# Kernel tuning notes

Hardware: AMD Instinct MI355X
Metric: run time of the kernel (lower is better)

The kernel has to match this reference:

```python
import jax, jax.numpy as jnp
import numpy as np

N_HEAD = 12
EPS_NORM = 1e-12   # F.normalize eps
EPS_DENOM = 1e-6   # clamp(min=1e-6)


def _l2norm(t):
    n = jnp.sqrt(jnp.sum(t * t, axis=-1, keepdims=True))
    return t / jnp.maximum(n, EPS_NORM)


def setup_inputs() -> dict:
    key = jax.random.key(0)
    ks = jax.random.split(key, 5)
    B, T, C = 1, 4096, 768
    x = jax.random.normal(ks[0], (B, T, C), dtype=jnp.float32)
    w_attn = jax.random.normal(ks[1], (C, 3 * C), dtype=jnp.float32) * 0.02
    b_attn = jnp.zeros((3 * C,), dtype=jnp.float32)
    w_proj = jax.random.normal(ks[2], (C, C), dtype=jnp.float32) * 0.02
    b_proj = jnp.zeros((C,), dtype=jnp.float32)
    return {"x": x, "w_attn": w_attn, "b_attn": b_attn,
            "w_proj": w_proj, "b_proj": b_proj}


def reference(x, w_attn, b_attn, w_proj, b_proj):
    B, T, C = x.shape
    H = N_HEAD
    hd = C // H
    qkv = x @ w_attn + b_attn                      # [B,T,3C]
    q, k, v = jnp.split(qkv, 3, axis=-1)
    # [B,T,C] -> [B,H,T,hd]
    def to_heads(t):
        return t.reshape(B, T, H, hd).transpose(0, 2, 1, 3)
    q, k, v = to_heads(q), to_heads(k), to_heads(v)
    # T > 512 branch: normalized-qk cumulative linear attention
    q = _l2norm(q)
    k = _l2norm(k)
    num = jnp.einsum('bhqd,bhkd->bhqk', q, k)      # [B,H,T,T]
    denom = jnp.maximum(jnp.cumsum(num, axis=-1), EPS_DENOM)
    att = num / denom
    y = jnp.einsum('bhqk,bhkd->bhqd', att, v)      # [B,H,T,hd]
    y = y.transpose(0, 2, 1, 3).reshape(B, T, C)
    return y @ w_proj + b_proj
```

## Files before the change

### kernel.cpp

```cpp
#include <hip/hip_runtime.h>

#define T_SEQ 4096
#define H_NUM 12
#define HD    64
#define C_DIM 768
#define N_QKV 2304
#define HT    (T_SEQ * HD)

typedef float    f32x4 __attribute__((ext_vector_type(4)));
typedef _Float16 half8 __attribute__((ext_vector_type(8)));
typedef _Float16 half4 __attribute__((ext_vector_type(4)));

#define GLDS(gp, lp) __builtin_amdgcn_global_load_lds( \
    (const __attribute__((address_space(1))) void*)(gp), \
    (__attribute__((address_space(3))) void*)(lp), 16, 0, 0)

__global__ __launch_bounds__(256) void split_x_kernel(
    const float* __restrict__ x, _Float16* __restrict__ xh,
    _Float16* __restrict__ xl, int n4)
{
    const int i = blockIdx.x * 256 + threadIdx.x;
    if (i >= n4) return;
    const float4 v = ((const float4*)x)[i];
    const float vv[4] = {v.x, v.y, v.z, v.w};
    half4 h, l;
    #pragma unroll
    for (int j = 0; j < 4; ++j) {
        const _Float16 hh = (_Float16)vv[j];
        h[j] = hh;
        l[j] = (_Float16)(vv[j] - (float)hh);
    }
    ((half4*)xh)[i] = h;
    ((half4*)xl)[i] = l;
}

__global__ __launch_bounds__(256) void split_wt_kernel(
    const float* __restrict__ W, _Float16* __restrict__ wth,
    _Float16* __restrict__ wtl)
{
    __shared__ float Ws[64][65];
    const int tid = threadIdx.x;
    const int n0 = blockIdx.x * 64, k0 = blockIdx.y * 64;
    const int lr = tid >> 4, lc = (tid & 15) << 2;
    #pragma unroll
    for (int i = 0; i < 4; ++i) {
        const float4 v = *(const float4*)(W + (size_t)(k0 + lr + i * 16) * N_QKV + n0 + lc);
        Ws[lr + i * 16][lc + 0] = v.x; Ws[lr + i * 16][lc + 1] = v.y;
        Ws[lr + i * 16][lc + 2] = v.z; Ws[lr + i * 16][lc + 3] = v.w;
    }
    __syncthreads();
    const int n = tid >> 2, ks = (tid & 3) << 4;
    half8 h0, h1, l0, l1;
    #pragma unroll
    for (int j = 0; j < 8; ++j) {
        const float v = Ws[ks + j][n];
        const _Float16 hh = (_Float16)v;
        h0[j] = hh; l0[j] = (_Float16)(v - (float)hh);
    }
    #pragma unroll
    for (int j = 0; j < 8; ++j) {
        const float v = Ws[ks + 8 + j][n];
        const _Float16 hh = (_Float16)v;
        h1[j] = hh; l1[j] = (_Float16)(v - (float)hh);
    }
    const size_t dst = (size_t)(n0 + n) * C_DIM + k0 + ks;
    *(half8*)(wth + dst) = h0; *(half8*)(wth + dst + 8) = h1;
    *(half8*)(wtl + dst) = l0; *(half8*)(wtl + dst + 8) = l1;
}

__global__ __launch_bounds__(256) void gemm_qkv_kernel(
    const _Float16* __restrict__ xh, const _Float16* __restrict__ xl,
    const _Float16* __restrict__ wth, const _Float16* __restrict__ wtl,
    const float* __restrict__ bias,
    _Float16* __restrict__ qhi, _Float16* __restrict__ qlo,
    _Float16* __restrict__ khi, _Float16* __restrict__ klo,
    _Float16* __restrict__ vt)
{
    __shared__ __align__(16) _Float16 AH[128 * 64];
    __shared__ __align__(16) _Float16 AL[128 * 64];
    __shared__ __align__(16) _Float16 BH[64 * 64];
    __shared__ __align__(16) _Float16 BL[64 * 64];
    const int tid = threadIdx.x;
    const int wv = tid >> 6, lane = tid & 63;
    const int fm = lane & 15, fg = lane >> 4;
    const int lrow = lane >> 3;
    const int lcs  = (lane & 7) ^ (lrow & 7);
    const int bx = blockIdx.x;
    const int m0 = blockIdx.y * 128;

    auto dma_chunk = [&](int c) {
        const int kc0 = c * 64;
        #pragma unroll
        for (int i = 0; i < 12; ++i) {
            const int qidx = wv * 12 + i;
            if (qidx < 16) {
                const int rg = qidx;
                GLDS(xh + (size_t)(m0 + rg * 8 + lrow) * C_DIM + kc0 + lcs * 8, &AH[rg * 512]);
            } else if (qidx < 32) {
                const int rg = qidx - 16;
                GLDS(xl + (size_t)(m0 + rg * 8 + lrow) * C_DIM + kc0 + lcs * 8, &AL[rg * 512]);
            } else if (qidx < 40) {
                const int rg = qidx - 32;
                GLDS(wth + (size_t)(bx * 64 + rg * 8 + lrow) * C_DIM + kc0 + lcs * 8, &BH[rg * 512]);
            } else {
                const int rg = qidx - 40;
                GLDS(wtl + (size_t)(bx * 64 + rg * 8 + lrow) * C_DIM + kc0 + lcs * 8, &BL[rg * 512]);
            }
        }
    };

    f32x4 acc[2][4];
    #pragma unroll
    for (int mt = 0; mt < 2; ++mt)
        #pragma unroll
        for (int ct = 0; ct < 4; ++ct) acc[mt][ct] = (f32x4){0.f, 0.f, 0.f, 0.f};

    const int swz = fm & 7;
    dma_chunk(0);
    #pragma unroll 1
    for (int c = 0; c < C_DIM / 64; ++c) {
        __syncthreads();
        half8 ah[2][2], al[2][2], bh[4][2], bl[4][2];
        #pragma unroll
        for (int mt = 0; mt < 2; ++mt) {
            const int rb = (wv * 32 + mt * 16 + fm) * 64;
            #pragma unroll
            for (int kc = 0; kc < 2; ++kc) {
                const int cb = ((kc * 4 + fg) ^ swz) * 8;
                ah[mt][kc] = *(const half8*)&AH[rb + cb];
                al[mt][kc] = *(const half8*)&AL[rb + cb];
            }
        }
        #pragma unroll
        for (int ct = 0; ct < 4; ++ct) {
            const int rb = (ct * 16 + fm) * 64;
            #pragma unroll
            for (int kc = 0; kc < 2; ++kc) {
                const int cb = ((kc * 4 + fg) ^ swz) * 8;
                bh[ct][kc] = *(const half8*)&BH[rb + cb];
                bl[ct][kc] = *(const half8*)&BL[rb + cb];
            }
        }
        __syncthreads();
        if (c + 1 < C_DIM / 64) dma_chunk(c + 1);
        #pragma unroll
        for (int mt = 0; mt < 2; ++mt)
            #pragma unroll
            for (int ct = 0; ct < 4; ++ct)
                #pragma unroll
                for (int kc = 0; kc < 2; ++kc) {
                    acc[mt][ct] = __builtin_amdgcn_mfma_f32_16x16x32_f16(ah[mt][kc], bh[ct][kc], acc[mt][ct], 0, 0, 0);
                    acc[mt][ct] = __builtin_amdgcn_mfma_f32_16x16x32_f16(ah[mt][kc], bl[ct][kc], acc[mt][ct], 0, 0, 0);
                    acc[mt][ct] = __builtin_amdgcn_mfma_f32_16x16x32_f16(al[mt][kc], bh[ct][kc], acc[mt][ct], 0, 0, 0);
                }
    }

    const int sec = bx / 12, h = bx % 12;
    const size_t hb = (size_t)h * HT;
    float bb[4];
    #pragma unroll
    for (int ct = 0; ct < 4; ++ct) bb[ct] = bias[bx * 64 + ct * 16 + fm];

    if (sec < 2) {
        _Float16* dh = (sec == 0) ? qhi : khi;
        _Float16* dl = (sec == 0) ? qlo : klo;
        #pragma unroll
        for (int mt = 0; mt < 2; ++mt)
            #pragma unroll
            for (int r = 0; r < 4; ++r) {
                float o[4];
                float ss = 0.f;
                #pragma unroll
                for (int ct = 0; ct < 4; ++ct) {
                    o[ct] = acc[mt][ct][r] + bb[ct];
                    ss += o[ct] * o[ct];
                }
                #pragma unroll
                for (int mk = 1; mk < 16; mk <<= 1) ss += __shfl_xor(ss, mk, 16);
                const float invn = 1.0f / fmaxf(sqrtf(ss), 1e-12f);
                const int t = m0 + wv * 32 + mt * 16 + fg * 4 + r;
                const size_t rb = hb + (size_t)t * HD;
                #pragma unroll
                for (int ct = 0; ct < 4; ++ct) {
                    const float v = o[ct] * invn;
                    const _Float16 vh = (_Float16)v;
                    dh[rb + ct * 16 + fm] = vh;
                    dl[rb + ct * 16 + fm] = (_Float16)(v - (float)vh);
                }
            }
    } else {
        #pragma unroll
        for (int mt = 0; mt < 2; ++mt) {
            const int t0 = m0 + wv * 32 + mt * 16 + fg * 4;
            #pragma unroll
            for (int ct = 0; ct < 4; ++ct) {
                half4 pk;
                #pragma unroll
                for (int r = 0; r < 4; ++r) pk[r] = (_Float16)(acc[mt][ct][r] + bb[ct]);
                *(half4*)(vt + hb + (size_t)(ct * 16 + fm) * T_SEQ + t0) = pk;
            }
        }
    }
}

__global__ __launch_bounds__(256) void attn_kernel(
    const _Float16* __restrict__ qhi, const _Float16* __restrict__ qlo,
    const _Float16* __restrict__ khi, const _Float16* __restrict__ klo,
    const _Float16* __restrict__ vt,  _Float16* __restrict__ ylin)
{
    __shared__ __align__(16) _Float16 KH[64 * 64];
    __shared__ __align__(16) _Float16 KL[64 * 64];
    __shared__ __align__(16) _Float16 VS[64 * 64];
    __shared__ __align__(16) _Float16 P2[64][72];

    const int tid = threadIdx.x;
    const int wv = tid >> 6, lane = tid & 63;
    const int fm = lane & 15, fg = lane >> 4;
    const int lrow = lane >> 3;
    const int lcs  = (lane & 7) ^ (lrow & 7);
    const int h = blockIdx.y, qt = blockIdx.x;
    const size_t hb = (size_t)h * HT;

    const int q = qt * 64 + wv * 16 + fm;
    half8 qf[2][2];
    #pragma unroll
    for (int kc = 0; kc < 2; ++kc) {
        const size_t off = hb + (size_t)q * HD + kc * 32 + fg * 8;
        qf[0][kc] = *(const half8*)(qhi + off);
        qf[1][kc] = *(const half8*)(qlo + off);
    }

    auto dma_tile = [&](int kt) {
        const size_t kb = hb + (size_t)kt * 64 * HD;
        const int vcol = kt * 64;
        #pragma unroll
        for (int i = 0; i < 6; ++i) {
            const int qidx = wv * 6 + i;
            const int rg = qidx & 7;
            if (qidx < 8) {
                GLDS(khi + kb + (size_t)(rg * 8 + lrow) * HD + lcs * 8, &KH[rg * 512]);
            } else if (qidx < 16) {
                GLDS(klo + kb + (size_t)(rg * 8 + lrow) * HD + lcs * 8, &KL[rg * 512]);
            } else {
                GLDS(vt + hb + (size_t)(rg * 8 + lrow) * T_SEQ + vcol + lcs * 8, &VS[rg * 512]);
            }
        }
    };

    f32x4 yacc[4];
    #pragma unroll
    for (int ct = 0; ct < 4; ++ct) yacc[ct] = (f32x4){0.f, 0.f, 0.f, 0.f};
    float carry = 0.0f;
    const int swz = fm & 7;

    dma_tile(0);
    #pragma unroll 1
    for (int kt = 0; kt < T_SEQ / 64; ++kt) {
        __syncthreads();
        half8 ka[4][2], kl[4][2], vf[4][2];
        #pragma unroll
        for (int kr = 0; kr < 4; ++kr) {
            const int rb = (kr * 16 + fm) * 64;
            #pragma unroll
            for (int kc = 0; kc < 2; ++kc) {
                const int cb = ((kc * 4 + fg) ^ swz) * 8;
                ka[kr][kc] = *(const half8*)&KH[rb + cb];
                kl[kr][kc] = *(const half8*)&KL[rb + cb];
            }
        }
        #pragma unroll
        for (int ct = 0; ct < 4; ++ct) {
            const int rb = (ct * 16 + fm) * 64;
            #pragma unroll
            for (int kc = 0; kc < 2; ++kc)
                vf[ct][kc] = *(const half8*)&VS[rb + (((kc * 4 + fg) ^ swz) * 8)];
        }
        __syncthreads();
        if (kt + 1 < T_SEQ / 64) dma_tile(kt + 1);

        f32x4 sacc[4];
        #pragma unroll
        for (int kr = 0; kr < 4; ++kr) sacc[kr] = (f32x4){0.f, 0.f, 0.f, 0.f};
        #pragma unroll
        for (int kr = 0; kr < 4; ++kr)
            #pragma unroll
            for (int kc = 0; kc < 2; ++kc) {
                sacc[kr] = __builtin_amdgcn_mfma_f32_16x16x32_f16(ka[kr][kc], qf[0][kc], sacc[kr], 0, 0, 0);
                sacc[kr] = __builtin_amdgcn_mfma_f32_16x16x32_f16(ka[kr][kc], qf[1][kc], sacc[kr], 0, 0, 0);
                sacc[kr] = __builtin_amdgcn_mfma_f32_16x16x32_f16(kl[kr][kc], qf[0][kc], sacc[kr], 0, 0, 0);
            }

        #pragma unroll
        for (int kr = 0; kr < 4; ++kr) {
            const float s0 = sacc[kr][0], s1 = sacc[kr][1];
            const float s2 = sacc[kr][2], s3 = sacc[kr][3];
            const float p1 = s0 + s1, p2 = p1 + s2, p3 = p2 + s3;
            const float u1 = __shfl_xor(p3, 16, 64);
            const float pair = p3 + u1;
            const float u2 = __shfl_xor(pair, 32, 64);
            const float tot16 = pair + u2;
            const float pref = ((fg & 1) ? u1 : 0.0f) + ((fg & 2) ? u2 : 0.0f);
            const float base = carry + pref;
            carry += tot16;
            const float a0 = s0 * __builtin_amdgcn_rcpf(fmaxf(base + s0, 1e-6f));
            const float a1 = s1 * __builtin_amdgcn_rcpf(fmaxf(base + p1, 1e-6f));
            const float a2 = s2 * __builtin_amdgcn_rcpf(fmaxf(base + p2, 1e-6f));
            const float a3 = s3 * __builtin_amdgcn_rcpf(fmaxf(base + p3, 1e-6f));
            half4 pk = {(_Float16)(a0 * 0.03125f), (_Float16)(a1 * 0.03125f),
                        (_Float16)(a2 * 0.03125f), (_Float16)(a3 * 0.03125f)};
            *(half4*)&P2[wv * 16 + fm][kr * 16 + fg * 4] = pk;
        }

        #pragma unroll
        for (int kc = 0; kc < 2; ++kc) {
            const half8 af = *(const half8*)&P2[wv * 16 + fm][kc * 32 + fg * 8];
            #pragma unroll
            for (int ct = 0; ct < 4; ++ct)
                yacc[ct] = __builtin_amdgcn_mfma_f32_16x16x32_f16(af, vf[ct][kc], yacc[ct], 0, 0, 0);
        }
    }

    #pragma unroll
    for (int ct = 0; ct < 4; ++ct)
        #pragma unroll
        for (int r = 0; r < 4; ++r) {
            const int t = qt * 64 + wv * 16 + fg * 4 + r;
            ylin[(size_t)t * C_DIM + h * HD + ct * 16 + fm] =
                (_Float16)(yacc[ct][r] * 0.0078125f);
        }
}

__global__ __launch_bounds__(256) void gemm_proj_kernel(
    const _Float16* __restrict__ A, const float* __restrict__ W,
    const float* __restrict__ bias, float* __restrict__ out)
{
    __shared__ _Float16 As[64][72];
    __shared__ _Float16 Bt[64][72];
    typedef _Float16 half2v __attribute__((ext_vector_type(2)));
    const int tid = threadIdx.x;
    const int w = tid >> 6, lane = tid & 63;
    const int m = lane & 15, g = lane >> 4;
    const int row0 = blockIdx.x << 6, col0 = blockIdx.y << 6;
    const int ar = tid >> 3, ac8 = (tid & 7) << 3;
    const int bn0 = (tid & 15) << 2, bpv = tid >> 4;
    f32x4 acc[4];
    #pragma unroll
    for (int ct = 0; ct < 4; ++ct) acc[ct] = (f32x4){0.f, 0.f, 0.f, 0.f};

    for (int kt = 0; kt < C_DIM; kt += 64) {
        half8 av0 = *(const half8*)(A + (size_t)(row0 + ar)      * C_DIM + kt + ac8);
        half8 av1 = *(const half8*)(A + (size_t)(row0 + ar + 32) * C_DIM + kt + ac8);
        float4 w0[2], w1[2];
        #pragma unroll
        for (int i = 0; i < 2; ++i) {
            const int k = kt + 2 * (bpv + 16 * i);
            w0[i] = *(const float4*)(W + (size_t)k       * C_DIM + col0 + bn0);
            w1[i] = *(const float4*)(W + (size_t)(k + 1) * C_DIM + col0 + bn0);
        }
        __syncthreads();
        *(half8*)&As[ar][ac8]      = av0;
        *(half8*)&As[ar + 32][ac8] = av1;
        #pragma unroll
        for (int i = 0; i < 2; ++i) {
            const int p = bpv + 16 * i;
            const float a_[4] = {w0[i].x, w0[i].y, w0[i].z, w0[i].w};
            const float b_[4] = {w1[i].x, w1[i].y, w1[i].z, w1[i].w};
            #pragma unroll
            for (int u = 0; u < 4; ++u) {
                half2v pk = {(_Float16)a_[u], (_Float16)b_[u]};
                *(half2v*)&Bt[bn0 + u][2 * p] = pk;
            }
        }
        __syncthreads();
        #pragma unroll
        for (int kc = 0; kc < 2; ++kc) {
            const half8 a = *(half8*)&As[w * 16 + m][kc * 32 + g * 8];
            #pragma unroll
            for (int ct = 0; ct < 4; ++ct) {
                const half8 b = *(half8*)&Bt[ct * 16 + m][kc * 32 + g * 8];
                acc[ct] = __builtin_amdgcn_mfma_f32_16x16x32_f16(a, b, acc[ct], 0, 0, 0);
            }
        }
    }
    #pragma unroll
    for (int ct = 0; ct < 4; ++ct)
        #pragma unroll
        for (int r = 0; r < 4; ++r) {
            const int t = row0 + w * 16 + g * 4 + r;
            const int n = col0 + ct * 16 + m;
            out[(size_t)t * C_DIM + n] = acc[ct][r] * 4096.0f + bias[n];
        }
}

extern "C" void kernel_launch(void* const* d_in, const int* in_sizes, int n_in,
                              void* d_out, int out_size, void* d_ws, size_t ws_size,
                              hipStream_t stream)
{
    const float* x      = (const float*)d_in[0];
    const float* w_attn = (const float*)d_in[1];
    const float* b_attn = (const float*)d_in[2];
    const float* w_proj = (const float*)d_in[3];
    const float* b_proj = (const float*)d_in[4];
    float* out = (float*)d_out;

    const size_t perQK = (size_t)H_NUM * HT;
    const size_t perX  = (size_t)T_SEQ * C_DIM;
    const size_t perW  = (size_t)N_QKV * C_DIM;
    _Float16* base = (_Float16*)d_ws;
    _Float16* xhi  = base;
    _Float16* xlo  = xhi + perX;
    _Float16* wthi = xlo + perX;
    _Float16* wtlo = wthi + perW;
    _Float16* qhi  = wtlo + perW;
    _Float16* qlo  = qhi + perQK;
    _Float16* khi  = qlo + perQK;
    _Float16* klo  = khi + perQK;
    _Float16* vtp  = klo + perQK;
    _Float16* ylin = xhi;

    split_x_kernel<<<(perX / 4 + 255) / 256, 256, 0, stream>>>(x, xhi, xlo, perX / 4);
    split_wt_kernel<<<dim3(N_QKV / 64, C_DIM / 64), 256, 0, stream>>>(w_attn, wthi, wtlo);
    gemm_qkv_kernel<<<dim3(N_QKV / 64, T_SEQ / 128), 256, 0, stream>>>(
        xhi, xlo, wthi, wtlo, b_attn, qhi, qlo, khi, klo, vtp);
    attn_kernel<<<dim3(T_SEQ / 64, H_NUM), 256, 0, stream>>>(
        qhi, qlo, khi, klo, vtp, ylin);
    gemm_proj_kernel<<<dim3(T_SEQ / 64, C_DIM / 64), 256, 0, stream>>>(
        ylin, w_proj, b_proj, out);
}
```

Before: 360.7 us.

## Split key range across waves using precomputed prefix key sums

Adds a kernel that computes per-head prefix sums of K over 64-key tiles. The attention kernel uses these to get each wave's starting cumulative denominator as q·Kprefix, so the four waves handle different key ranges in parallel over all 64 queries instead of each wave walking all 4096 keys serially. Partial outputs are reduced through LDS at the end. The cost is dropping the shared-memory K/V staging and DMA prefetch in favour of direct global loads, plus higher register pressure from the 4x4 accumulator arrays.

```diff
diff --git a/kernel.cpp b/kernel.cpp
--- a/kernel.cpp
+++ b/kernel.cpp
@@ -203,131 +203,204 @@
     }
 }
 
-__global__ __launch_bounds__(256) void attn_kernel(
+__global__ __launch_bounds__(1024) void ksp_kernel(
+    const _Float16* __restrict__ khi, const _Float16* __restrict__ klo,
+    _Float16* __restrict__ ksphi, _Float16* __restrict__ ksplo)
+{
+    __shared__ float TS[64][64];
+    const int h = blockIdx.x;
+    const int d = threadIdx.x & 63, seg = threadIdx.x >> 6;
+    const _Float16* bh = khi + (size_t)h * HT;
+    const _Float16* bl = klo + (size_t)h * HT;
+    #pragma unroll 1
+    for (int j = 0; j < 4; ++j) {
+        const int kt = seg * 4 + j;
+        float s = 0.f;
+        #pragma unroll 4
+        for (int k = 0; k < 64; ++k) {
+            const size_t key = (size_t)kt * 64 + k;
+            s += (float)bh[key * HD + d] + (float)bl[key * HD + d];
+        }
+        TS[kt][d] = s;
+    }
+    __syncthreads();
+    if (threadIdx.x < 64) {
+        float cum = 0.f;
+        #pragma unroll 1
+        for (int kt = 0; kt < 64; ++kt) {
+            const _Float16 hi = (_Float16)cum;
+            const size_t o = ((size_t)h * 64 + kt) * 64 + d;
+            ksphi[o] = hi;
+            ksplo[o] = (_Float16)(cum - (float)hi);
+            cum += TS[kt][d];
+        }
+    }
+}
+
+__global__ __launch_bounds__(256, 2) void attn_kernel(
     const _Float16* __restrict__ qhi, const _Float16* __restrict__ qlo,
     const _Float16* __restrict__ khi, const _Float16* __restrict__ klo,
-    const _Float16* __restrict__ vt,  _Float16* __restrict__ ylin)
-{
-    __shared__ __align__(16) _Float16 KH[64 * 64];
-    __shared__ __align__(16) _Float16 KL[64 * 64];
-    __shared__ __align__(16) _Float16 VS[64 * 64];
-    __shared__ __align__(16) _Float16 P2[64][72];
-
+    const _Float16* __restrict__ vt,
+    const _Float16* __restrict__ ksphi, const _Float16* __restrict__ ksplo,
+    _Float16* __restrict__ ylin)
+{
+    __shared__ __align__(16) _Float16 P2[4][64][72];
     const int tid = threadIdx.x;
     const int wv = tid >> 6, lane = tid & 63;
     const int fm = lane & 15, fg = lane >> 4;
-    const int lrow = lane >> 3;
-    const int lcs  = (lane & 7) ^ (lrow & 7);
     const int h = blockIdx.y, qt = blockIdx.x;
     const size_t hb = (size_t)h * HT;
 
-    const int q = qt * 64 + wv * 16 + fm;
-    half8 qf[2][2];
-    #pragma unroll
-    for (int kc = 0; kc < 2; ++kc) {
-        const size_t off = hb + (size_t)q * HD + kc * 32 + fg * 8;
-        qf[0][kc] = *(const half8*)(qhi + off);
-        qf[1][kc] = *(const half8*)(qlo + off);
-    }
-
-    auto dma_tile = [&](int kt) {
-        const size_t kb = hb + (size_t)kt * 64 * HD;
-        const int vcol = kt * 64;
-        #pragma unroll
-        for (int i = 0; i < 6; ++i) {
-            const int qidx = wv * 6 + i;
-            const int rg = qidx & 7;
-            if (qidx < 8) {
-                GLDS(khi + kb + (size_t)(rg * 8 + lrow) * HD + lcs * 8, &KH[rg * 512]);
-            } else if (qidx < 16) {
-                GLDS(klo + kb + (size_t)(rg * 8 + lrow) * HD + lcs * 8, &KL[rg * 512]);
-            } else {
-                GLDS(vt + hb + (size_t)(rg * 8 + lrow) * T_SEQ + vcol + lcs * 8, &VS[rg * 512]);
-            }
-        }
-    };
-
-    f32x4 yacc[4];
-    #pragma unroll
-    for (int ct = 0; ct < 4; ++ct) yacc[ct] = (f32x4){0.f, 0.f, 0.f, 0.f};
-    float carry = 0.0f;
-    const int swz = fm & 7;
-
-    dma_tile(0);
+    half8 qf[4][2][2];
+    #pragma unroll
+    for (int s = 0; s < 4; ++s)
+        #pragma unroll
+        for (int kc = 0; kc < 2; ++kc) {
+            const size_t off = hb + (size_t)(qt * 64 + s * 16 + fm) * HD + kc * 32 + fg * 8;
+            qf[s][0][kc] = *(const half8*)(qhi + off);
+            qf[s][1][kc] = *(const half8*)(qlo + off);
+        }
+
+    f32x4 basv[4];
+    {
+        const _Float16* sh = ksphi + (size_t)h * 4096;
+        const _Float16* sl = ksplo + (size_t)h * 4096;
+        #pragma unroll
+        for (int kr = 0; kr < 4; ++kr) {
+            half8 kh_[2], kl_[2];
+            #pragma unroll
+            for (int kc = 0; kc < 2; ++kc) {
+                const size_t o = (size_t)(kr * 16 + fm) * 64 + kc * 32 + fg * 8;
+                kh_[kc] = *(const half8*)(sh + o);
+                kl_[kc] = *(const half8*)(sl + o);
+            }
+            #pragma unroll
+            for (int s = 0; s < 4; ++s) {
+                f32x4 b = (f32x4){0.f, 0.f, 0.f, 0.f};
+                #pragma unroll
+                for (int kc = 0; kc < 2; ++kc) {
+                    b = __builtin_amdgcn_mfma_f32_16x16x32_f16(kh_[kc], qf[s][0][kc], b, 0, 0, 0);
+                    b = __builtin_amdgcn_mfma_f32_16x16x32_f16(kh_[kc], qf[s][1][kc], b, 0, 0, 0);
+                    b = __builtin_amdgcn_mfma_f32_16x16x32_f16(kl_[kc], qf[s][0][kc], b, 0, 0, 0);
+                }
+                basv[s][kr] = (wv == 0) ? b[0] : (wv == 1) ? b[1] : (wv == 2) ? b[2] : b[3];
+            }
+        }
+    }
+
+    f32x4 yacc[4][4];
+    #pragma unroll
+    for (int s = 0; s < 4; ++s)
+        #pragma unroll
+        for (int ct = 0; ct < 4; ++ct) yacc[s][ct] = (f32x4){0.f, 0.f, 0.f, 0.f};
+
     #pragma unroll 1
-    for (int kt = 0; kt < T_SEQ / 64; ++kt) {
+    for (int it = 0; it < 16; ++it) {
+        const int i4 = it >> 2, itf = it & 3;
+        const int key0 = (it * 4 + wv) * 64;
+        const size_t kb = hb + (size_t)key0 * HD;
+
+        half8 ka[4][2], kl2[4][2];
+        #pragma unroll
+        for (int kr = 0; kr < 4; ++kr)
+            #pragma unroll
+            for (int kc = 0; kc < 2; ++kc) {
+                const size_t o = kb + (size_t)(kr * 16 + fm) * HD + kc * 32 + fg * 8;
+                ka[kr][kc]  = *(const half8*)(khi + o);
+                kl2[kr][kc] = *(const half8*)(klo + o);
+            }
+
+        f32x4 sacc[4][4];
+        #pragma unroll
+        for (int s = 0; s < 4; ++s)
+            #pragma unroll
+            for (int kr = 0; kr < 4; ++kr) sacc[s][kr] = (f32x4){0.f, 0.f, 0.f, 0.f};
+        #pragma unroll
+        for (int kr = 0; kr < 4; ++kr)
+            #pragma unroll
+            for (int s = 0; s < 4; ++s)
+                #pragma unroll
+                for (int kc = 0; kc < 2; ++kc) {
+                    sacc[s][kr] = __builtin_amdgcn_mfma_f32_16x16x32_f16(ka[kr][kc],  qf[s][0][kc], sacc[s][kr], 0, 0, 0);
+                    sacc[s][kr] = __builtin_amdgcn_mfma_f32_16x16x32_f16(ka[kr][kc],  qf[s][1][kc], sacc[s][kr], 0, 0, 0);
+                    sacc[s][kr] = __builtin_amdgcn_mfma_f32_16x16x32_f16(kl2[kr][kc], qf[s][0][kc], sacc[s][kr], 0, 0, 0);
+                }
+
+        half8 vf[4][2];
+        #pragma unroll
+        for (int ct = 0; ct < 4; ++ct)
+            #pragma unroll
+            for (int kc = 0; kc < 2; ++kc)
+                vf[ct][kc] = *(const half8*)(vt + hb + (size_t)(ct * 16 + fm) * T_SEQ
+                                             + key0 + kc * 32 + fg * 8);
+
+        #pragma unroll
+        for (int s = 0; s < 4; ++s) {
+            const f32x4 bq = basv[s];
+            const float bsel = (i4 == 0) ? bq[0] : (i4 == 1) ? bq[1] : (i4 == 2) ? bq[2] : bq[3];
+            float loc = __shfl(bsel, itf * 16 + fm, 64);
+            #pragma unroll
+            for (int kr = 0; kr < 4; ++kr) {
+                const float s0 = sacc[s][kr][0], s1 = sacc[s][kr][1];
+                const float s2 = sacc[s][kr][2], s3 = sacc[s][kr][3];
+                const float p1 = s0 + s1, p2 = p1 + s2, p3 = p2 + s3;
+                const float u1 = __shfl_xor(p3, 16, 64);
+                const float pair = p3 + u1;
+                const float u2 = __shfl_xor(pair, 32, 64);
+                const float tot16 = pair + u2;
+                const float pref = ((fg & 1) ? u1 : 0.0f) + ((fg & 2) ? u2 : 0.0f);
+                const float base = loc + pref;
+                loc += tot16;
+                const float a0 = s0 * __builtin_amdgcn_rcpf(fmaxf(base + s0, 1e-6f));
+                const float a1 = s1 * __builtin_amdgcn_rcpf(fmaxf(base + p1, 1e-6f));
+                const float a2 = s2 * __builtin_amdgcn_rcpf(fmaxf(base + p2, 1e-6f));
+                const float a3 = s3 * __builtin_amdgcn_rcpf(fmaxf(base + p3, 1e-6f));
+                half4 pk = {(_Float16)(a0 * 0.03125f), (_Float16)(a1 * 0.03125f),
+                            (_Float16)(a2 * 0.03125f), (_Float16)(a3 * 0.03125f)};
+                *(half4*)&P2[wv][s * 16 + fm][kr * 16 + fg * 4] = pk;
+            }
+        }
+
+        #pragma unroll
+        for (int s = 0; s < 4; ++s)
+            #pragma unroll
+            for (int kc = 0; kc < 2; ++kc) {
+                const half8 af = *(const half8*)&P2[wv][s * 16 + fm][kc * 32 + fg * 8];
+                #pragma unroll
+                for (int ct = 0; ct < 4; ++ct)
+                    yacc[s][ct] = __builtin_amdgcn_mfma_f32_16x16x32_f16(af, vf[ct][kc], yacc[s][ct], 0, 0, 0);
+            }
+    }
+
+    __syncthreads();
+    float* YR = (float*)&P2[0][0][0];
+    #pragma unroll 1
+    for (int w = 0; w < 4; ++w) {
+        if (wv == w) {
+            #pragma unroll
+            for (int s = 0; s < 4; ++s)
+                #pragma unroll
+                for (int ct = 0; ct < 4; ++ct)
+                    #pragma unroll
+                    for (int r = 0; r < 4; ++r) {
+                        const int qq = s * 16 + fg * 4 + r, dv = ct * 16 + fm;
+                        if (w == 0) YR[qq * 66 + dv]  = yacc[s][ct][r];
+                        else        YR[qq * 66 + dv] += yacc[s][ct][r];
+                    }
+        }
         __syncthreads();
-        half8 ka[4][2], kl[4][2], vf[4][2];
-        #pragma unroll
-        for (int kr = 0; kr < 4; ++kr) {
-            const int rb = (kr * 16 + fm) * 64;
-            #pragma unroll
-            for (int kc = 0; kc < 2; ++kc) {
-                const int cb = ((kc * 4 + fg) ^ swz) * 8;
-                ka[kr][kc] = *(const half8*)&KH[rb + cb];
-                kl[kr][kc] = *(const half8*)&KL[rb + cb];
-            }
-        }
-        #pragma unroll
-        for (int ct = 0; ct < 4; ++ct) {
-            const int rb = (ct * 16 + fm) * 64;
-            #pragma unroll
-            for (int kc = 0; kc < 2; ++kc)
-                vf[ct][kc] = *(const half8*)&VS[rb + (((kc * 4 + fg) ^ swz) * 8)];
-        }
-        __syncthreads();
-        if (kt + 1 < T_SEQ / 64) dma_tile(kt + 1);
-
-        f32x4 sacc[4];
-        #pragma unroll
-        for (int kr = 0; kr < 4; ++kr) sacc[kr] = (f32x4){0.f, 0.f, 0.f, 0.f};
-        #pragma unroll
-        for (int kr = 0; kr < 4; ++kr)
-            #pragma unroll
-            for (int kc = 0; kc < 2; ++kc) {
-                sacc[kr] = __builtin_amdgcn_mfma_f32_16x16x32_f16(ka[kr][kc], qf[0][kc], sacc[kr], 0, 0, 0);
-                sacc[kr] = __builtin_amdgcn_mfma_f32_16x16x32_f16(ka[kr][kc], qf[1][kc], sacc[kr], 0, 0, 0);
-                sacc[kr] = __builtin_amdgcn_mfma_f32_16x16x32_f16(kl[kr][kc], qf[0][kc], sacc[kr], 0, 0, 0);
-            }
-
-        #pragma unroll
-        for (int kr = 0; kr < 4; ++kr) {
-            const float s0 = sacc[kr][0], s1 = sacc[kr][1];
-            const float s2 = sacc[kr][2], s3 = sacc[kr][3];
-            const float p1 = s0 + s1, p2 = p1 + s2, p3 = p2 + s3;
-            const float u1 = __shfl_xor(p3, 16, 64);
-            const float pair = p3 + u1;
-            const float u2 = __shfl_xor(pair, 32, 64);
-            const float tot16 = pair + u2;
-            const float pref = ((fg & 1) ? u1 : 0.0f) + ((fg & 2) ? u2 : 0.0f);
-            const float base = carry + pref;
-            carry += tot16;
-            const float a0 = s0 * __builtin_amdgcn_rcpf(fmaxf(base + s0, 1e-6f));
-            const float a1 = s1 * __builtin_amdgcn_rcpf(fmaxf(base + p1, 1e-6f));
-            const float a2 = s2 * __builtin_amdgcn_rcpf(fmaxf(base + p2, 1e-6f));
-            const float a3 = s3 * __builtin_amdgcn_rcpf(fmaxf(base + p3, 1e-6f));
-            half4 pk = {(_Float16)(a0 * 0.03125f), (_Float16)(a1 * 0.03125f),
-                        (_Float16)(a2 * 0.03125f), (_Float16)(a3 * 0.03125f)};
-            *(half4*)&P2[wv * 16 + fm][kr * 16 + fg * 4] = pk;
-        }
-
-        #pragma unroll
-        for (int kc = 0; kc < 2; ++kc) {
-            const half8 af = *(const half8*)&P2[wv * 16 + fm][kc * 32 + fg * 8];
-            #pragma unroll
-            for (int ct = 0; ct < 4; ++ct)
-                yacc[ct] = __builtin_amdgcn_mfma_f32_16x16x32_f16(af, vf[ct][kc], yacc[ct], 0, 0, 0);
-        }
-    }
-
-    #pragma unroll
-    for (int ct = 0; ct < 4; ++ct)
-        #pragma unroll
-        for (int r = 0; r < 4; ++r) {
-            const int t = qt * 64 + wv * 16 + fg * 4 + r;
-            ylin[(size_t)t * C_DIM + h * HD + ct * 16 + fm] =
-                (_Float16)(yacc[ct][r] * 0.0078125f);
-        }
+    }
+    const int tq = tid >> 2, c0 = (tid & 3) * 16;
+    const float* yr = &YR[tq * 66 + c0];
+    half8 o0, o1;
+    #pragma unroll
+    for (int j = 0; j < 8; ++j) {
+        o0[j] = (_Float16)(yr[j]     * 0.0078125f);
+        o1[j] = (_Float16)(yr[8 + j] * 0.0078125f);
+    }
+    _Float16* dst = ylin + (size_t)(qt * 64 + tq) * C_DIM + h * HD + c0;
+    *(half8*)dst       = o0;
+    *(half8*)(dst + 8) = o1;
 }
 
 __global__ __launch_bounds__(256) void gemm_proj_kernel(
@@ -417,13 +490,16 @@
     _Float16* klo  = khi + perQK;
     _Float16* vtp  = klo + perQK;
     _Float16* ylin = xhi;
+    _Float16* ksph = xlo;
+    _Float16* kspl = xlo + (size_t)H_NUM * 64 * 64;
 
     split_x_kernel<<<(perX / 4 + 255) / 256, 256, 0, stream>>>(x, xhi, xlo, perX / 4);
     split_wt_kernel<<<dim3(N_QKV / 64, C_DIM / 64), 256, 0, stream>>>(w_attn, wthi, wtlo);
     gemm_qkv_kernel<<<dim3(N_QKV / 64, T_SEQ / 128), 256, 0, stream>>>(
         xhi, xlo, wthi, wtlo, b_attn, qhi, qlo, khi, klo, vtp);
+    ksp_kernel<<<H_NUM, 1024, 0, stream>>>(khi, klo, ksph, kspl);
     attn_kernel<<<dim3(T_SEQ / 64, H_NUM), 256, 0, stream>>>(
-        qhi, qlo, khi, klo, vtp, ylin);
+        qhi, qlo, khi, klo, vtp, ksph, kspl, ylin);
     gemm_proj_kernel<<<dim3(T_SEQ / 64, C_DIM / 64), 256, 0, stream>>>(
         ylin, w_proj, b_proj, out);
 }
```

New measurement: 438.9 us. 21.7% more time.
